# Kernel tuning notes

Hardware: AMD Instinct MI355X
Metric: run time of the kernel (lower is better)

## Reference

```python
import jax, jax.numpy as jnp
import numpy as np

N = 40000   # nodes
E2 = 320000  # undirected edge pairs (640k directed)
C = 128      # in = out channels


def _lap_matvec(x, row, col, dinv):
    # (L~ x)_i = -sum_{j in N(i)} d_i^{-1/2} d_j^{-1/2} x_j   (sym norm, lambda_max=2 -> zero diag)
    w = -(dinv[row] * dinv[col])                       # [E]
    return jax.ops.segment_sum(w[:, None] * x[col], row, num_segments=x.shape[0])


def _cheb_conv(x, row, col, dinv, W0, W1, b):
    # K=2 Chebyshev: Tx_0 = x, Tx_1 = L~ x
    return x @ W0 + _lap_matvec(x, row, col, dinv) @ W1 + b


def setup_inputs() -> dict:
    key = jax.random.key(0)
    ks = jax.random.split(key, 8)
    x = jax.random.normal(ks[0], (N, C), dtype=jnp.float32)
    ei = jax.random.randint(ks[1], (2, E2), 0, N)
    edge_index = jnp.concatenate([ei, ei[::-1]], axis=1)  # symmetric graph [2, 2*E2]
    s = 1.0 / np.sqrt(C)
    W00 = jax.random.normal(ks[2], (C, C), dtype=jnp.float32) * s
    W01 = jax.random.normal(ks[3], (C, C), dtype=jnp.float32) * s
    b0 = jnp.zeros((C,), dtype=jnp.float32)
    W10 = jax.random.normal(ks[4], (C, C), dtype=jnp.float32) * s
    W11 = jax.random.normal(ks[5], (C, C), dtype=jnp.float32) * s
    b1 = jnp.zeros((C,), dtype=jnp.float32)
    return {"x": x, "edge_index": edge_index, "W00": W00, "W01": W01, "b0": b0,
            "W10": W10, "W11": W11, "b1": b1}


def reference(x, edge_index, W00, W01, b0, W10, W11, b1):
    row, col = edge_index[0], edge_index[1]
    deg = jax.ops.segment_sum(jnp.ones(row.shape, dtype=x.dtype), row, num_segments=x.shape[0])
    dinv = jnp.where(deg > 0, jax.lax.rsqrt(jnp.maximum(deg, 1.0)), 0.0)
    y = jax.nn.relu(_cheb_conv(x, row, col, dinv, W00, W01, b0))
    y = jax.nn.relu(_cheb_conv(y, row, col, dinv, W10, W11, b1))
    return (x + y) * 0.5
```

## Files before the change

### kernel.cpp

```cpp
#include <hip/hip_runtime.h>

#define CH 128

typedef unsigned int uint;
typedef unsigned short ushort;
typedef unsigned char uchar;
typedef __attribute__((ext_vector_type(8))) short bf16x8;
typedef __attribute__((ext_vector_type(4))) float f32x4;
typedef __attribute__((ext_vector_type(2))) float f32x2;

__device__ inline ushort f2bf(float f) {
    uint u = __float_as_uint(f);
    u += 0x7fffu + ((u >> 16) & 1u);
    return (ushort)(u >> 16);
}
__device__ inline uint pk(float a, float b) { return (uint)f2bf(a) | ((uint)f2bf(b) << 16); }

#if defined(__has_builtin)
#if __has_builtin(__builtin_amdgcn_cvt_pk_f32_fp8) && __has_builtin(__builtin_amdgcn_cvt_pk_fp8_f32)
#define HAVE_FP8_CVT 1
#endif
#endif

__device__ inline uint f32_to_fp8_manual(float f) {
    uint u = __float_as_uint(f);
    uint s = (u >> 24) & 0x80u;
    float a = fabsf(f);
    if (a < 0x1.0p-10f) return s;
    if (a >= 448.f) return s | 0x7eu;
    if (a < 0x1.0p-6f) {
        uint m = (uint)(a * 512.f + 0.5f);
        return s | m;
    }
    uint au = u & 0x7fffffffu;
    uint r = au + 0x7ffffu + ((au >> 20) & 1u);
    uint e = (r >> 23) - 120u;
    return s | (e << 3) | ((r >> 20) & 7u);
}
__device__ inline float fp8_to_f32_manual(uint b) {
    uint s = (b & 0x80u) << 24;
    uint em = (b & 0x7fu) << 20;
    return __uint_as_float(s | em) * 0x1.0p+120f;
}
__device__ inline uint pk_fp8x4(float a, float b, float c, float d) {
#ifdef HAVE_FP8_CVT
    uint r = __builtin_amdgcn_cvt_pk_fp8_f32(a, b, 0u, false);
    r = __builtin_amdgcn_cvt_pk_fp8_f32(c, d, r, true);
    return r;
#else
    return f32_to_fp8_manual(a) | (f32_to_fp8_manual(b) << 8) |
           (f32_to_fp8_manual(c) << 16) | (f32_to_fp8_manual(d) << 24);
#endif
}
__device__ inline uchar f2fp8(float a) {
#ifdef HAVE_FP8_CVT
    return (uchar)(__builtin_amdgcn_cvt_pk_fp8_f32(a, a, 0u, false) & 0xffu);
#else
    return (uchar)f32_to_fp8_manual(a);
#endif
}
__device__ inline void fp8x4_acc(uint v, f32x2& a01, f32x2& a23) {
#ifdef HAVE_FP8_CVT
    f32x2 p0 = __builtin_amdgcn_cvt_pk_f32_fp8((int)v, false);
    f32x2 p1 = __builtin_amdgcn_cvt_pk_f32_fp8((int)v, true);
    a01 += p0; a23 += p1;
#else
    a01[0] += fp8_to_f32_manual(v & 0xffu);
    a01[1] += fp8_to_f32_manual((v >> 8) & 0xffu);
    a23[0] += fp8_to_f32_manual((v >> 16) & 0xffu);
    a23[1] += fp8_to_f32_manual(v >> 24);
#endif
}

#define CSR_CAP 64

__global__ void k_prolog(const float* __restrict__ W00, const float* __restrict__ W01,
                         const float* __restrict__ W10, const float* __restrict__ W11,
                         uint* __restrict__ Wt0, uint* __restrict__ Wt1,
                         int* __restrict__ deg, int N) {
    if (blockIdx.x < 128) {
        int tid = blockIdx.x * 256 + threadIdx.x;
        int which = tid >> 14;
        int t = tid & 16383;
        int col = t & 127, kp = t >> 7;
        int k = kp * 2;
        const float* W = (which == 0) ? ((k < 128) ? W00 : W01) : ((k < 128) ? W10 : W11);
        uint* Wt = (which == 0) ? Wt0 : Wt1;
        int kk = k & 127;
        float f0 = W[(size_t)kk * 128 + col];
        float f1 = W[(size_t)(kk + 1) * 128 + col];
        Wt[(size_t)col * 128 + kp] = pk(f0, f1);
    } else {
        int i = (blockIdx.x - 128) * 256 + threadIdx.x;
        if (i < N) deg[i] = 0;
    }
}

__global__ void k_deg(const int* __restrict__ row, int* __restrict__ deg,
                      int* __restrict__ pos, int E) {
    int e = blockIdx.x * blockDim.x + threadIdx.x;
    if (e < E) pos[e] = atomicAdd(&deg[row[e]], 1);
}

__global__ void k_big(const float4* __restrict__ X, const int* __restrict__ deg,
                      uint2* __restrict__ Xb, uint* __restrict__ Xsb,
                      const int* __restrict__ row, const int* __restrict__ col,
                      const int* __restrict__ pos, int* __restrict__ csr,
                      int n4, int E, int cvtB) {
    if ((int)blockIdx.x < cvtB) {
        int i = blockIdx.x * 256 + threadIdx.x;
        if (i >= n4) return;
        float4 v = X[i];
        int d = deg[i >> 5];
        float s = (d > 0) ? rsqrtf((float)d) : 0.0f;
        Xb[i]  = make_uint2(pk(v.x, v.y), pk(v.z, v.w));
        Xsb[i] = pk_fp8x4(v.x * s, v.y * s, v.z * s, v.w * s);
    } else {
        int e = ((int)blockIdx.x - cvtB) * 256 + threadIdx.x;
        if (e < E) {
            int p = pos[e];
            if (p < CSR_CAP) csr[(size_t)row[e] * CSR_CAP + p] = col[e];
        }
    }
}

__global__ __launch_bounds__(256) void k_fused(const uint* __restrict__ A1,
                                               const uint* __restrict__ Xs,
                                               const uint* __restrict__ Wt,
                                               const float* __restrict__ bias,
                                               const float* __restrict__ xres,
                                               const int* __restrict__ deg,
                                               const int* __restrict__ csr,
                                               void* __restrict__ outp,
                                               uchar* __restrict__ outs,
                                               int N, int mode) {
    __shared__ uint LxT[64 * 68];
    __shared__ uint AsU[2][64 * 20];
    __shared__ uint WsU[2][128 * 20];

    const int tid = threadIdx.x;
    const int row0 = blockIdx.x * 64;

    const int sra = tid >> 2;
    const int sca = tid & 3;
    const uint4* A1p = (const uint4*)A1;
    const uint4* Wtp = (const uint4*)Wt;
    const int arow = row0 + sra;
    const int idx1 = tid + 256;
    uint4 ga  = A1p[(size_t)arow * 16 + sca];
    uint4 gw0 = Wtp[(size_t)sra * 32 + sca];
    uint4 gw1 = Wtp[(size_t)(idx1 >> 2) * 32 + (idx1 & 3)];
    *(uint4*)&AsU[0][sra * 20 + sca * 4] = ga;
    *(uint4*)&WsU[0][sra * 20 + sca * 4] = gw0;
    *(uint4*)&WsU[0][(idx1 >> 2) * 20 + (idx1 & 3) * 4] = gw1;

    {
        const int hw = tid >> 5;
        const int l = tid & 31;
        for (int rr = 0; rr < 8; ++rr) {
            const int r = row0 + hw * 8 + rr;
            const int d = min(deg[r], CSR_CAP);
            const int* cp = csr + (size_t)r * CSR_CAP;
            f32x2 a01 = {0.f, 0.f}, a23 = {0.f, 0.f};
            int k = 0;
            for (; k + 8 <= d; k += 8) {
                int j0 = cp[k+0], j1 = cp[k+1], j2 = cp[k+2], j3 = cp[k+3];
                int j4 = cp[k+4], j5 = cp[k+5], j6 = cp[k+6], j7 = cp[k+7];
                uint v0 = Xs[(size_t)j0 * 32 + l];
                uint v1 = Xs[(size_t)j1 * 32 + l];
                uint v2 = Xs[(size_t)j2 * 32 + l];
                uint v3 = Xs[(size_t)j3 * 32 + l];
                uint v4 = Xs[(size_t)j4 * 32 + l];
                uint v5 = Xs[(size_t)j5 * 32 + l];
                uint v6 = Xs[(size_t)j6 * 32 + l];
                uint v7 = Xs[(size_t)j7 * 32 + l];
                fp8x4_acc(v0, a01, a23); fp8x4_acc(v1, a01, a23);
                fp8x4_acc(v2, a01, a23); fp8x4_acc(v3, a01, a23);
                fp8x4_acc(v4, a01, a23); fp8x4_acc(v5, a01, a23);
                fp8x4_acc(v6, a01, a23); fp8x4_acc(v7, a01, a23);
            }
            for (; k + 4 <= d; k += 4) {
                int j0 = cp[k+0], j1 = cp[k+1], j2 = cp[k+2], j3 = cp[k+3];
                uint v0 = Xs[(size_t)j0 * 32 + l];
                uint v1 = Xs[(size_t)j1 * 32 + l];
                uint v2 = Xs[(size_t)j2 * 32 + l];
                uint v3 = Xs[(size_t)j3 * 32 + l];
                fp8x4_acc(v0, a01, a23); fp8x4_acc(v1, a01, a23);
                fp8x4_acc(v2, a01, a23); fp8x4_acc(v3, a01, a23);
            }
            for (; k < d; ++k) {
                uint v = Xs[(size_t)cp[k] * 32 + l];
                fp8x4_acc(v, a01, a23);
            }
            float sc = (d > 0) ? -rsqrtf((float)d) : 0.f;
            *(uint2*)&LxT[(hw * 8 + rr) * 68 + 2 * l] =
                make_uint2(pk(a01[0] * sc, a01[1] * sc), pk(a23[0] * sc, a23[1] * sc));
        }
    }
    __syncthreads();

    const int lane = tid & 63;
    const int wid = tid >> 6;
    const int wr = wid >> 1;
    const int wc = wid & 1;
    const int l16 = lane & 15;
    const int lk = lane >> 4;

    f32x4 acc[2][4];
    #pragma unroll
    for (int m = 0; m < 2; m++)
        #pragma unroll
        for (int n = 0; n < 4; n++)
            acc[m][n] = (f32x4){0.f, 0.f, 0.f, 0.f};

    for (int t = 0; t < 8; ++t) {
        const int cur = t & 1;
        if (t < 7) {
            const int k0 = (t + 1) * 32;
            if (k0 < 128) ga = A1p[(size_t)arow * 16 + (k0 >> 3) + sca];
            gw0 = Wtp[(size_t)sra * 32 + (k0 >> 3) + sca];
            gw1 = Wtp[(size_t)(idx1 >> 2) * 32 + (k0 >> 3) + (idx1 & 3)];
        }

        bf16x8 bfr[4];
        #pragma unroll
        for (int n = 0; n < 4; n++) {
            int colc = wc * 64 + n * 16 + l16;
            bfr[n] = *(const bf16x8*)&WsU[cur][colc * 20 + lk * 4];
        }
        #pragma unroll
        for (int m = 0; m < 2; m++) {
            int rowc = wr * 32 + m * 16 + l16;
            bf16x8 afr = (t < 4)
                ? *(const bf16x8*)&AsU[cur][rowc * 20 + lk * 4]
                : *(const bf16x8*)&LxT[rowc * 68 + (t - 4) * 16 + lk * 4];
            #pragma unroll
            for (int n = 0; n < 4; n++)
                acc[m][n] = __builtin_amdgcn_mfma_f32_16x16x32_bf16(afr, bfr[n], acc[m][n], 0, 0, 0);
        }

        if (t < 7) {
            if (t + 1 < 4) *(uint4*)&AsU[cur ^ 1][sra * 20 + sca * 4] = ga;
            *(uint4*)&WsU[cur ^ 1][sra * 20 + sca * 4] = gw0;
            *(uint4*)&WsU[cur ^ 1][(idx1 >> 2) * 20 + (idx1 & 3) * 4] = gw1;
            __syncthreads();
        }
    }

    if (mode == 0) {
        ushort* O = (ushort*)outp;
        #pragma unroll
        for (int m = 0; m < 2; m++) {
            #pragma unroll
            for (int r = 0; r < 4; r++) {
                int rg = row0 + wr * 32 + m * 16 + lk * 4 + r;
                int d = deg[rg];
                float sc = (d > 0) ? rsqrtf((float)d) : 0.f;
                #pragma unroll
                for (int n = 0; n < 4; n++) {
                    const int colc = wc * 64 + n * 16 + l16;
                    float v = fmaxf(acc[m][n][r] + bias[colc], 0.f);
                    O[(size_t)rg * 128 + colc] = f2bf(v);
                    outs[(size_t)rg * 128 + colc] = f2fp8(v * sc);
                }
            }
        }
    } else {
        float* O = (float*)outp;
        #pragma unroll
        for (int m = 0; m < 2; m++) {
            #pragma unroll
            for (int r = 0; r < 4; r++) {
                int rg = row0 + wr * 32 + m * 16 + lk * 4 + r;
                #pragma unroll
                for (int n = 0; n < 4; n++) {
                    const int colc = wc * 64 + n * 16 + l16;
                    float v = fmaxf(acc[m][n][r] + bias[colc], 0.f);
                    O[(size_t)rg * 128 + colc] = 0.5f * (v + xres[(size_t)rg * 128 + colc]);
                }
            }
        }
    }
}

extern "C" void kernel_launch(void* const* d_in, const int* in_sizes, int n_in,
                              void* d_out, int out_size, void* d_ws, size_t ws_size,
                              hipStream_t stream) {
    const float* x   = (const float*)d_in[0];
    const int*   ei  = (const int*)d_in[1];
    const float* W00 = (const float*)d_in[2];
    const float* W01 = (const float*)d_in[3];
    const float* b0  = (const float*)d_in[4];
    const float* W10 = (const float*)d_in[5];
    const float* W11 = (const float*)d_in[6];
    const float* b1  = (const float*)d_in[7];
    float* out = (float*)d_out;

    const int N = in_sizes[0] / CH;
    const int E = in_sizes[1] / 2;
    const int* row = ei;
    const int* col = ei + E;

    char* ws = (char*)d_ws;
    size_t off = 0;
    auto alloc = [&](size_t bytes) -> void* {
        void* p = ws + off;
        off += (bytes + 255) & ~(size_t)255;
        return p;
    };
    int*   deg = (int*)alloc((size_t)N * 4);
    int*   pos = (int*)alloc((size_t)E * 4);
    int*   csr = (int*)alloc((size_t)N * CSR_CAP * 4);
    uint*  xb  = (uint*)alloc((size_t)N * 64 * 4);
    uint*  xsb = (uint*)alloc((size_t)N * 32 * 4);
    uint*  yb  = (uint*)alloc((size_t)N * 64 * 4);
    uchar* ysb = (uchar*)alloc((size_t)N * 128);
    uint*  Wt0 = (uint*)alloc(128 * 128 * 4);
    uint*  Wt1 = (uint*)alloc(128 * 128 * 4);

    const int nB   = (N + 255) / 256;
    const int n4   = N * 32;
    const int cvtB = (n4 + 255) / 256;
    const int filB = (E + 255) / 256;

    k_prolog<<<128 + nB, 256, 0, stream>>>(W00, W01, W10, W11, Wt0, Wt1, deg, N);
    k_deg<<<filB, 256, 0, stream>>>(row, deg, pos, E);
    k_big<<<cvtB + filB, 256, 0, stream>>>((const float4*)x, deg,
                                           (uint2*)xb, xsb, row, col, pos, csr,
                                           n4, E, cvtB);

    const int fusedBlocks = (N + 63) / 64;

    k_fused<<<fusedBlocks, 256, 0, stream>>>(xb, xsb, Wt0, b0, nullptr, deg, csr,
                                             (void*)yb, ysb, N, 0);
    k_fused<<<fusedBlocks, 256, 0, stream>>>(yb, (const uint*)ysb, Wt1, b1, x, deg, csr,
                                             (void*)out, nullptr, N, 1);
}
```

Measured before the change: 128.8 us.

## Split fused SpMM+GEMM into separate kernels and merge degree count with CSR fill

Merges the degree atomic and the CSR fill into one kernel by using the atomicAdd return value as the slot directly, which removes the pos buffer and one pass over the edges. The fused gather+GEMM kernel is split into a standalone SpMM kernel, one row per 32 lanes, that writes the bf16 Laplacian product to a new global buffer. A pure MFMA GEMM kernel then streams both operands through the double-buffered LDS pipeline. This trades extra global traffic and more launches for higher occupancy and better load balance in the gather phase, which no longer sits behind the GEMM's LDS use. Row bounds checks are added for the case where N is not a multiple of the tile size.

```diff
diff --git a/kernel.cpp b/kernel.cpp
--- a/kernel.cpp
+++ b/kernel.cpp
@@ -1,6 +1,7 @@
 #include <hip/hip_runtime.h>
 
 #define CH 128
+#define CSR_CAP 64
 
 typedef unsigned int uint;
 typedef unsigned short ushort;
@@ -71,8 +72,6 @@
     a23[1] += fp8_to_f32_manual(v >> 24);
 #endif
 }
-
-#define CSR_CAP 64
 
 __global__ void k_prolog(const float* __restrict__ W00, const float* __restrict__ W01,
                          const float* __restrict__ W10, const float* __restrict__ W11,
@@ -96,113 +95,77 @@
     }
 }
 
-__global__ void k_deg(const int* __restrict__ row, int* __restrict__ deg,
-                      int* __restrict__ pos, int E) {
+__global__ void k_degfill(const int* __restrict__ row, const int* __restrict__ col,
+                          int* __restrict__ deg, int* __restrict__ csr, int E) {
     int e = blockIdx.x * blockDim.x + threadIdx.x;
-    if (e < E) pos[e] = atomicAdd(&deg[row[e]], 1);
-}
-
-__global__ void k_big(const float4* __restrict__ X, const int* __restrict__ deg,
-                      uint2* __restrict__ Xb, uint* __restrict__ Xsb,
-                      const int* __restrict__ row, const int* __restrict__ col,
-                      const int* __restrict__ pos, int* __restrict__ csr,
-                      int n4, int E, int cvtB) {
-    if ((int)blockIdx.x < cvtB) {
-        int i = blockIdx.x * 256 + threadIdx.x;
-        if (i >= n4) return;
-        float4 v = X[i];
-        int d = deg[i >> 5];
-        float s = (d > 0) ? rsqrtf((float)d) : 0.0f;
-        Xb[i]  = make_uint2(pk(v.x, v.y), pk(v.z, v.w));
-        Xsb[i] = pk_fp8x4(v.x * s, v.y * s, v.z * s, v.w * s);
-    } else {
-        int e = ((int)blockIdx.x - cvtB) * 256 + threadIdx.x;
-        if (e < E) {
-            int p = pos[e];
-            if (p < CSR_CAP) csr[(size_t)row[e] * CSR_CAP + p] = col[e];
-        }
-    }
-}
-
-__global__ __launch_bounds__(256) void k_fused(const uint* __restrict__ A1,
-                                               const uint* __restrict__ Xs,
-                                               const uint* __restrict__ Wt,
-                                               const float* __restrict__ bias,
-                                               const float* __restrict__ xres,
-                                               const int* __restrict__ deg,
-                                               const int* __restrict__ csr,
-                                               void* __restrict__ outp,
-                                               uchar* __restrict__ outs,
-                                               int N, int mode) {
-    __shared__ uint LxT[64 * 68];
+    if (e < E) {
+        int r = row[e];
+        int p = atomicAdd(&deg[r], 1);
+        if (p < CSR_CAP) csr[(size_t)r * CSR_CAP + p] = col[e];
+    }
+}
+
+__global__ void k_cvt(const float4* __restrict__ X, const int* __restrict__ deg,
+                      uint2* __restrict__ Xb, uint* __restrict__ Xsb, int n4) {
+    int i = blockIdx.x * 256 + threadIdx.x;
+    if (i >= n4) return;
+    float4 v = X[i];
+    int d = deg[i >> 5];
+    float s = (d > 0) ? rsqrtf((float)d) : 0.0f;
+    Xb[i]  = make_uint2(pk(v.x, v.y), pk(v.z, v.w));
+    Xsb[i] = pk_fp8x4(v.x * s, v.y * s, v.z * s, v.w * s);
+}
+
+__global__ __launch_bounds__(256) void k_spmm(const uint* __restrict__ Xs,
+                                              const int* __restrict__ deg,
+                                              const int* __restrict__ csr,
+                                              uint2* __restrict__ Ob, int N) {
+    int r = (int)((blockIdx.x * 256 + threadIdx.x) >> 5);
+    int l = threadIdx.x & 31;
+    if (r >= N) return;
+    int d = min(deg[r], CSR_CAP);
+    const int* cp = csr + (size_t)r * CSR_CAP;
+    const uint* X = Xs + l;
+    f32x2 a01 = {0.f, 0.f}, a23 = {0.f, 0.f};
+    int k = 0;
+    for (; k + 4 <= d; k += 4) {
+        int j0 = cp[k + 0], j1 = cp[k + 1], j2 = cp[k + 2], j3 = cp[k + 3];
+        uint v0 = X[(size_t)j0 * 32];
+        uint v1 = X[(size_t)j1 * 32];
+        uint v2 = X[(size_t)j2 * 32];
+        uint v3 = X[(size_t)j3 * 32];
+        fp8x4_acc(v0, a01, a23);
+        fp8x4_acc(v1, a01, a23);
+        fp8x4_acc(v2, a01, a23);
+        fp8x4_acc(v3, a01, a23);
+    }
+    for (; k < d; ++k) {
+        uint v = X[(size_t)cp[k] * 32];
+        fp8x4_acc(v, a01, a23);
+    }
+    float sc = (d > 0) ? -rsqrtf((float)d) : 0.f;
+    Ob[(size_t)r * 32 + l] = make_uint2(pk(a01[0] * sc, a01[1] * sc),
+                                        pk(a23[0] * sc, a23[1] * sc));
+}
+
+__global__ __launch_bounds__(256) void k_gemm_mfma(const uint* __restrict__ A1,
+                                                   const uint* __restrict__ A2,
+                                                   const uint* __restrict__ Wt,
+                                                   const float* __restrict__ bias,
+                                                   const float* __restrict__ xres,
+                                                   const int* __restrict__ deg,
+                                                   void* __restrict__ outp,
+                                                   uchar* __restrict__ outs,
+                                                   int N, int mode) {
     __shared__ uint AsU[2][64 * 20];
     __shared__ uint WsU[2][128 * 20];
 
     const int tid = threadIdx.x;
-    const int row0 = blockIdx.x * 64;
-
-    const int sra = tid >> 2;
-    const int sca = tid & 3;
-    const uint4* A1p = (const uint4*)A1;
-    const uint4* Wtp = (const uint4*)Wt;
-    const int arow = row0 + sra;
-    const int idx1 = tid + 256;
-    uint4 ga  = A1p[(size_t)arow * 16 + sca];
-    uint4 gw0 = Wtp[(size_t)sra * 32 + sca];
-    uint4 gw1 = Wtp[(size_t)(idx1 >> 2) * 32 + (idx1 & 3)];
-    *(uint4*)&AsU[0][sra * 20 + sca * 4] = ga;
-    *(uint4*)&WsU[0][sra * 20 + sca * 4] = gw0;
-    *(uint4*)&WsU[0][(idx1 >> 2) * 20 + (idx1 & 3) * 4] = gw1;
-
-    {
-        const int hw = tid >> 5;
-        const int l = tid & 31;
-        for (int rr = 0; rr < 8; ++rr) {
-            const int r = row0 + hw * 8 + rr;
-            const int d = min(deg[r], CSR_CAP);
-            const int* cp = csr + (size_t)r * CSR_CAP;
-            f32x2 a01 = {0.f, 0.f}, a23 = {0.f, 0.f};
-            int k = 0;
-            for (; k + 8 <= d; k += 8) {
-                int j0 = cp[k+0], j1 = cp[k+1], j2 = cp[k+2], j3 = cp[k+3];
-                int j4 = cp[k+4], j5 = cp[k+5], j6 = cp[k+6], j7 = cp[k+7];
-                uint v0 = Xs[(size_t)j0 * 32 + l];
-                uint v1 = Xs[(size_t)j1 * 32 + l];
-                uint v2 = Xs[(size_t)j2 * 32 + l];
-                uint v3 = Xs[(size_t)j3 * 32 + l];
-                uint v4 = Xs[(size_t)j4 * 32 + l];
-                uint v5 = Xs[(size_t)j5 * 32 + l];
-                uint v6 = Xs[(size_t)j6 * 32 + l];
-                uint v7 = Xs[(size_t)j7 * 32 + l];
-                fp8x4_acc(v0, a01, a23); fp8x4_acc(v1, a01, a23);
-                fp8x4_acc(v2, a01, a23); fp8x4_acc(v3, a01, a23);
-                fp8x4_acc(v4, a01, a23); fp8x4_acc(v5, a01, a23);
-                fp8x4_acc(v6, a01, a23); fp8x4_acc(v7, a01, a23);
-            }
-            for (; k + 4 <= d; k += 4) {
-                int j0 = cp[k+0], j1 = cp[k+1], j2 = cp[k+2], j3 = cp[k+3];
-                uint v0 = Xs[(size_t)j0 * 32 + l];
-                uint v1 = Xs[(size_t)j1 * 32 + l];
-                uint v2 = Xs[(size_t)j2 * 32 + l];
-                uint v3 = Xs[(size_t)j3 * 32 + l];
-                fp8x4_acc(v0, a01, a23); fp8x4_acc(v1, a01, a23);
-                fp8x4_acc(v2, a01, a23); fp8x4_acc(v3, a01, a23);
-            }
-            for (; k < d; ++k) {
-                uint v = Xs[(size_t)cp[k] * 32 + l];
-                fp8x4_acc(v, a01, a23);
-            }
-            float sc = (d > 0) ? -rsqrtf((float)d) : 0.f;
-            *(uint2*)&LxT[(hw * 8 + rr) * 68 + 2 * l] =
-                make_uint2(pk(a01[0] * sc, a01[1] * sc), pk(a23[0] * sc, a23[1] * sc));
-        }
-    }
-    __syncthreads();
-
     const int lane = tid & 63;
     const int wid = tid >> 6;
     const int wr = wid >> 1;
     const int wc = wid & 1;
+    const int row0 = blockIdx.x * 64;
     const int l16 = lane & 15;
     const int lk = lane >> 4;
 
@@ -212,13 +175,35 @@
         #pragma unroll
         for (int n = 0; n < 4; n++)
             acc[m][n] = (f32x4){0.f, 0.f, 0.f, 0.f};
+
+    const int sra = tid >> 2;
+    const int sca = tid & 3;
+    const uint4* A1p = (const uint4*)A1;
+    const uint4* A2p = (const uint4*)A2;
+    const uint4* Wtp = (const uint4*)Wt;
+    const int arow = min(row0 + sra, N - 1);
+
+    uint4 ga, gw0, gw1;
+    ga  = A1p[(size_t)arow * 16 + sca];
+    {
+        int idx0 = tid, idx1 = tid + 256;
+        gw0 = Wtp[(size_t)(idx0 >> 2) * 32 + (idx0 & 3)];
+        gw1 = Wtp[(size_t)(idx1 >> 2) * 32 + (idx1 & 3)];
+        *(uint4*)&AsU[0][sra * 20 + sca * 4] = ga;
+        *(uint4*)&WsU[0][(idx0 >> 2) * 20 + (idx0 & 3) * 4] = gw0;
+        *(uint4*)&WsU[0][(idx1 >> 2) * 20 + (idx1 & 3) * 4] = gw1;
+    }
+    __syncthreads();
 
     for (int t = 0; t < 8; ++t) {
         const int cur = t & 1;
         if (t < 7) {
             const int k0 = (t + 1) * 32;
-            if (k0 < 128) ga = A1p[(size_t)arow * 16 + (k0 >> 3) + sca];
-            gw0 = Wtp[(size_t)sra * 32 + (k0 >> 3) + sca];
+            const uint4* Ap = (k0 < 128) ? A1p : A2p;
+            const int kk = k0 & 127;
+            ga  = Ap[(size_t)arow * 16 + (kk >> 3) + sca];
+            int idx0 = tid, idx1 = tid + 256;
+            gw0 = Wtp[(size_t)(idx0 >> 2) * 32 + (k0 >> 3) + (idx0 & 3)];
             gw1 = Wtp[(size_t)(idx1 >> 2) * 32 + (k0 >> 3) + (idx1 & 3)];
         }
 
@@ -231,17 +216,16 @@
         #pragma unroll
         for (int m = 0; m < 2; m++) {
             int rowc = wr * 32 + m * 16 + l16;
-            bf16x8 afr = (t < 4)
-                ? *(const bf16x8*)&AsU[cur][rowc * 20 + lk * 4]
-                : *(const bf16x8*)&LxT[rowc * 68 + (t - 4) * 16 + lk * 4];
+            bf16x8 afr = *(const bf16x8*)&AsU[cur][rowc * 20 + lk * 4];
             #pragma unroll
             for (int n = 0; n < 4; n++)
                 acc[m][n] = __builtin_amdgcn_mfma_f32_16x16x32_bf16(afr, bfr[n], acc[m][n], 0, 0, 0);
         }
 
         if (t < 7) {
-            if (t + 1 < 4) *(uint4*)&AsU[cur ^ 1][sra * 20 + sca * 4] = ga;
-            *(uint4*)&WsU[cur ^ 1][sra * 20 + sca * 4] = gw0;
+            int idx0 = tid, idx1 = tid + 256;
+            *(uint4*)&AsU[cur ^ 1][sra * 20 + sca * 4] = ga;
+            *(uint4*)&WsU[cur ^ 1][(idx0 >> 2) * 20 + (idx0 & 3) * 4] = gw0;
             *(uint4*)&WsU[cur ^ 1][(idx1 >> 2) * 20 + (idx1 & 3) * 4] = gw1;
             __syncthreads();
         }
@@ -254,6 +238,7 @@
             #pragma unroll
             for (int r = 0; r < 4; r++) {
                 int rg = row0 + wr * 32 + m * 16 + lk * 4 + r;
+                if (rg >= N) continue;
                 int d = deg[rg];
                 float sc = (d > 0) ? rsqrtf((float)d) : 0.f;
                 #pragma unroll
@@ -272,6 +257,7 @@
             #pragma unroll
             for (int r = 0; r < 4; r++) {
                 int rg = row0 + wr * 32 + m * 16 + lk * 4 + r;
+                if (rg >= N) continue;
                 #pragma unroll
                 for (int n = 0; n < 4; n++) {
                     const int colc = wc * 64 + n * 16 + l16;
@@ -309,10 +295,10 @@
         return p;
     };
     int*   deg = (int*)alloc((size_t)N * 4);
-    int*   pos = (int*)alloc((size_t)E * 4);
     int*   csr = (int*)alloc((size_t)N * CSR_CAP * 4);
     uint*  xb  = (uint*)alloc((size_t)N * 64 * 4);
     uint*  xsb = (uint*)alloc((size_t)N * 32 * 4);
+    uint*  Lb  = (uint*)alloc((size_t)N * 64 * 4);
     uint*  yb  = (uint*)alloc((size_t)N * 64 * 4);
     uchar* ysb = (uchar*)alloc((size_t)N * 128);
     uint*  Wt0 = (uint*)alloc(128 * 128 * 4);
@@ -324,15 +310,17 @@
     const int filB = (E + 255) / 256;
 
     k_prolog<<<128 + nB, 256, 0, stream>>>(W00, W01, W10, W11, Wt0, Wt1, deg, N);
-    k_deg<<<filB, 256, 0, stream>>>(row, deg, pos, E);
-    k_big<<<cvtB + filB, 256, 0, stream>>>((const float4*)x, deg,
-                                           (uint2*)xb, xsb, row, col, pos, csr,
-                                           n4, E, cvtB);
-
-    const int fusedBlocks = (N + 63) / 64;
-
-    k_fused<<<fusedBlocks, 256, 0, stream>>>(xb, xsb, Wt0, b0, nullptr, deg, csr,
-                                             (void*)yb, ysb, N, 0);
-    k_fused<<<fusedBlocks, 256, 0, stream>>>(yb, (const uint*)ysb, Wt1, b1, x, deg, csr,
-                                             (void*)out, nullptr, N, 1);
-}
+    k_degfill<<<filB, 256, 0, stream>>>(row, col, deg, csr, E);
+    k_cvt<<<cvtB, 256, 0, stream>>>((const float4*)x, deg, (uint2*)xb, xsb, n4);
+
+    const int gemmBlocks = (N + 63) / 64;
+    const int spmmBlocks = (N * 32 + 255) / 256;
+
+    k_spmm<<<spmmBlocks, 256, 0, stream>>>(xsb, deg, csr, (uint2*)Lb, N);
+    k_gemm_mfma<<<gemmBlocks, 256, 0, stream>>>(xb, Lb, Wt0, b0, nullptr, deg,
+                                                (void*)yb, ysb, N, 0);
+
+    k_spmm<<<spmmBlocks, 256, 0, stream>>>((const uint*)ysb, deg, csr, (uint2*)Lb, N);
+    k_gemm_mfma<<<gemmBlocks, 256, 0, stream>>>(yb, Lb, Wt1, b1, x, deg,
+                                                (void*)out, nullptr, N, 1);
+}
```

Result: faster. 110.3 us (-14.4%).
